# Optimization experiments

Hardware: AMD Instinct MI355X
Metric: run time of the kernel (lower is better)

## Reference

```python
import jax, jax.numpy as jnp
import numpy as np
from jax import lax

R = 4                      # search_range
FILTERS = [128, 128, 96, 64, 32, 2]
B, H, W, C = 8, 128, 128, 128
IN_CH = (2 * R + 1) ** 2 + C + 2   # 81 + 128 + 2 = 211


def mish(x):
    return x * jnp.tanh(jax.nn.softplus(x))


def sepconv(x, dw, pw, b=None, act=True):
    # depthwise 3x3 (SAME) then pointwise 1x1, matching SeparableConv2D
    cin = x.shape[-1]
    y = lax.conv_general_dilated(
        x, dw, window_strides=(1, 1), padding='SAME',
        dimension_numbers=('NHWC', 'HWIO', 'NHWC'),
        feature_group_count=cin)
    y = jnp.einsum('bhwc,co->bhwo', y, pw)
    if b is not None:
        y = y + b
    return mish(y) if act else y


def warp(img, flo):
    # bilinear backward warp; TF casts float->int32 with truncation, jnp matches
    b_, h, w, _ = img.shape
    xs = jnp.arange(w, dtype=jnp.float32)[None, None, :]
    ys = jnp.arange(h, dtype=jnp.float32)[None, :, None]
    x = xs + flo[..., 0]
    y = ys + flo[..., 1]
    x0 = x.astype(jnp.int32)
    y0 = y.astype(jnp.int32)
    x1 = x0 + 1
    y1 = y0 + 1
    x0c = jnp.clip(x0, 0, w - 1)
    x1c = jnp.clip(x1, 0, w - 1)
    y0c = jnp.clip(y0, 0, h - 1)
    y1c = jnp.clip(y1, 0, h - 1)
    bi = jnp.arange(b_)[:, None, None]
    Ia = img[bi, y0c, x0c]
    Ib = img[bi, y1c, x0c]
    Ic = img[bi, y0c, x1c]
    Id = img[bi, y1c, x1c]
    x0f = x0c.astype(jnp.float32); x1f = x1c.astype(jnp.float32)
    y0f = y0c.astype(jnp.float32); y1f = y1c.astype(jnp.float32)
    wa = ((x1f - x) * (y1f - y))[..., None]
    wb = ((x1f - x) * (y - y0f))[..., None]
    wc = ((x - x0f) * (y1f - y))[..., None]
    wd = ((x - x0f) * (y - y0f))[..., None]
    return wa * Ia + wb * Ib + wc * Ic + wd * Id


def cost_volume(prv, nxt):
    _, h, w, _ = prv.shape
    d = 2 * R + 1
    pad = jnp.pad(nxt, ((0, 0), (R, R), (R, R), (0, 0)))
    costs = [jnp.mean(prv * pad[:, i:i + h, j:j + w, :], axis=-1)
             for i in range(d) for j in range(d)]
    return jnp.stack(costs, axis=-1)  # [B,H,W,81]


def setup_inputs() -> dict:
    key = jax.random.key(0)
    ks = iter(jax.random.split(key, 64))
    inp = {
        'prv': jax.random.normal(next(ks), (B, H, W, C), dtype=jnp.float32),
        'nxt': jax.random.normal(next(ks), (B, H, W, C), dtype=jnp.float32),
        'flo': jax.random.normal(next(ks), (B, H, W, 2), dtype=jnp.float32),
    }
    cin = IN_CH
    for i, f in enumerate(FILTERS):
        inp[f'dw{i}'] = 0.05 * jax.random.normal(next(ks), (3, 3, 1, cin), dtype=jnp.float32)
        inp[f'pw{i}'] = 0.05 * jax.random.normal(next(ks), (cin, f), dtype=jnp.float32)
        if i < len(FILTERS) - 1:
            inp[f'b{i}'] = 0.05 * jax.random.normal(next(ks), (f,), dtype=jnp.float32)
        cin = f
    return inp


def reference(prv, nxt, flo,
              dw0, pw0, b0, dw1, pw1, b1, dw2, pw2, b2,
              dw3, pw3, b3, dw4, pw4, b4, dw5, pw5):
    nxt_w = warp(nxt, flo)
    cost = cost_volume(prv, nxt_w)
    x = jnp.concatenate([cost, prv, flo], axis=-1)  # [B,H,W,211]
    x = sepconv(x, dw0, pw0, b0)
    x = sepconv(x, dw1, pw1, b1)
    x = sepconv(x, dw2, pw2, b2)
    x = sepconv(x, dw3, pw3, b3)
    x = sepconv(x, dw4, pw4, b4)
    x = sepconv(x, dw5, pw5, None, act=False)  # final flow, no bias/activation
    return x
```

## Files before the change

kernel.cpp:

```cpp
#include <hip/hip_runtime.h>
#include <hip/hip_bf16.h>

#define B_ 8
#define H_ 128
#define W_ 128
#define C_ 128

using f32x4 = __attribute__((ext_vector_type(4))) float;
using s16x8 = __attribute__((ext_vector_type(8))) short;
using us4   = __attribute__((ext_vector_type(4))) unsigned short;

__device__ __forceinline__ float mish_f(float x) {
    float t = __expf(fminf(x, 20.0f));
    float u = t * (t + 2.0f);
    return x * u / (u + 2.0f);
}

__device__ __forceinline__ int swz_row(int blk) {
    return ((blk & 7) << 7) | (blk >> 3);
}

__device__ __forceinline__ unsigned short f2bf_rne(float x) {
    unsigned u = __builtin_bit_cast(unsigned, x);
    u += 0x7FFFu + ((u >> 16) & 1u);
    return (unsigned short)(u >> 16);
}
__device__ __forceinline__ float bf2f(unsigned short h) {
    unsigned u = ((unsigned)h) << 16;
    return __builtin_bit_cast(float, u);
}
__device__ __forceinline__ unsigned short f2bf_hw(float x) {
    return __bfloat16_as_ushort(__float2bfloat16(x));
}

__device__ __forceinline__ f32x4 load4u(const float* p) {
    f32x4 v;
    __builtin_memcpy(&v, p, 16);
    return v;
}

__global__ __launch_bounds__(256) void warp_kernel(
    const float* __restrict__ nxt, const float* __restrict__ flo,
    float* __restrict__ nxtw)
{
    const int tid = threadIdx.x;
    const int c   = tid & 127;
    const int pix = blockIdx.x * 2 + (tid >> 7);
    const int b   = pix >> 14;
    const int rem = pix & 16383;
    const int y   = rem >> 7;
    const int x   = rem & 127;

    const float fx = flo[(size_t)pix * 2 + 0];
    const float fy = flo[(size_t)pix * 2 + 1];
    const float xf = (float)x + fx;
    const float yf = (float)y + fy;
    const int x0 = (int)xf;
    const int y0 = (int)yf;
    const int x0c = min(max(x0, 0), W_ - 1);
    const int x1c = min(max(x0 + 1, 0), W_ - 1);
    const int y0c = min(max(y0, 0), H_ - 1);
    const int y1c = min(max(y0 + 1, 0), H_ - 1);
    const float x0f = (float)x0c, x1f = (float)x1c;
    const float y0f = (float)y0c, y1f = (float)y1c;
    const float wa = (x1f - xf) * (y1f - yf);
    const float wb = (x1f - xf) * (yf - y0f);
    const float wc = (xf - x0f) * (y1f - yf);
    const float wd = (xf - x0f) * (yf - y0f);

    const float* base = nxt + (size_t)b * H_ * W_ * C_;
    const float Ia = base[((size_t)y0c * W_ + x0c) * C_ + c];
    const float Ib = base[((size_t)y1c * W_ + x0c) * C_ + c];
    const float Ic = base[((size_t)y0c * W_ + x1c) * C_ + c];
    const float Id = base[((size_t)y1c * W_ + x1c) * C_ + c];
    nxtw[(size_t)pix * C_ + c] = wa * Ia + wb * Ib + wc * Ic + wd * Id;
}

__global__ __launch_bounds__(1024, 4) void costvol_mfma_kernel(
    const float* __restrict__ prv, const float* __restrict__ nxtw,
    float* __restrict__ cost)
{
    constexpr int NSTR = 40;
    __shared__ unsigned short Nhi[2][144 * NSTR];
    __shared__ unsigned short Nlo[2][144 * NSTR];
    __shared__ float scr[8][512];

    const int tid  = threadIdx.x;
    const int lane = tid & 63;
    const int wv   = tid >> 6;
    const int w    = wv >> 1;
    const int nt   = wv & 1;
    const int r    = swz_row(blockIdx.x);
    const int y    = r & 127;
    const int b    = r >> 7;
    const int ko   = (lane >> 4) * 8;
    const int m15  = lane & 15;

    auto stageN = [&](int q, int kt, int bb) {
        if (q < 0 || q >= H_) return;
        const float* nb = nxtw + ((size_t)(b * H_ + q) * W_) * C_ + kt * 32;
        #pragma unroll
        for (int p = 0; p < 2; ++p) {
            const int idx = tid + 1024 * p;
            if (p == 0 || tid < 128) {
                const int sm = idx >> 3;
                const int c4 = (idx & 7) * 4;
                const int gx = sm - 8;
                float4 v = make_float4(0.f, 0.f, 0.f, 0.f);
                if (gx >= 0 && gx < W_)
                    v = *(const float4*)&nb[(size_t)gx * C_ + c4];
                us4 hv, lv;
                #pragma unroll
                for (int j = 0; j < 4; ++j) {
                    const float f = ((const float*)&v)[j];
                    const unsigned short hh = f2bf_hw(f);
                    hv[j] = hh;
                    lv[j] = f2bf_hw(f - bf2f(hh));
                }
                *(us4*)&Nhi[bb][sm * NSTR + c4] = hv;
                *(us4*)&Nlo[bb][sm * NSTR + c4] = lv;
            }
        }
    };

    f32x4 acc[9];
    #pragma unroll
    for (int d = 0; d < 9; ++d) acc[d] = (f32x4){0.f, 0.f, 0.f, 0.f};

    const float* pbase = prv + ((size_t)r * W_ + (w * 16 + m15)) * C_;
    float4 pf0 = *(const float4*)&pbase[ko];
    float4 pf1 = *(const float4*)&pbase[ko + 4];

    stageN(y - 4, 0, 0);
    __syncthreads();

    int cur = 0;
    s16x8 ahi, alo;
    for (int kt = 0; kt < 4; ++kt) {
        #pragma unroll
        for (int d = 0; d < 9; ++d) {
            if (d == 0) {
                #pragma unroll
                for (int j = 0; j < 8; ++j) {
                    const float f = (j < 4) ? ((const float*)&pf0)[j]
                                            : ((const float*)&pf1)[j - 4];
                    const unsigned short hh = f2bf_hw(f);
                    ahi[j] = (short)hh;
                    alo[j] = (short)f2bf_hw(f - bf2f(hh));
                }
            }
            if (d == 5 && kt < 3) {
                pf0 = *(const float4*)&pbase[(kt + 1) * 32 + ko];
                pf1 = *(const float4*)&pbase[(kt + 1) * 32 + ko + 4];
            }
            {
                const int nkt = (d == 8) ? kt + 1 : kt;
                const int nd  = (d == 8) ? 0 : d + 1;
                if (nkt < 4) stageN(y + nd - 4, nkt, cur ^ 1);
            }
            const int q = y + d - 4;
            if (q >= 0 && q < H_) {
                const int boff = (w * 16 + nt * 16 + m15) * NSTR + ko;
                const s16x8 bhi = *(const s16x8*)&Nhi[cur][boff];
                const s16x8 blo = *(const s16x8*)&Nlo[cur][boff];
                acc[d] = __builtin_amdgcn_mfma_f32_16x16x32_bf16(alo, bhi, acc[d], 0, 0, 0);
                acc[d] = __builtin_amdgcn_mfma_f32_16x16x32_bf16(ahi, blo, acc[d], 0, 0, 0);
                acc[d] = __builtin_amdgcn_mfma_f32_16x16x32_bf16(ahi, bhi, acc[d], 0, 0, 0);
            }
            __syncthreads();
            cur ^= 1;
        }
    }

    const int quad = lane >> 4;
    #pragma unroll
    for (int d = 0; d < 9; ++d) {
        #pragma unroll
        for (int g = 0; g < 4; ++g)
            scr[w][(quad * 4 + g) * 32 + nt * 16 + m15] = acc[d][g];
        __syncthreads();
        #pragma unroll
        for (int p = 0; p < 2; ++p) {
            const int idx = tid + 1024 * p;
            if (p == 0 || tid < 128) {
                const int x  = idx / 9;
                const int dx = idx - x * 9;
                const int ww = x >> 4, m = x & 15;
                const float v = scr[ww][m * 32 + m + dx + 4] * (1.0f / 128.0f);
                cost[((size_t)r * W_ + x) * 81 + d * 9 + dx] = v;
            }
        }
        __syncthreads();
    }
}

__global__ __launch_bounds__(256) void prep_kernel(
    const float* __restrict__ pw, int CIN, int COUT, int NT,
    unsigned short* __restrict__ hi, unsigned short* __restrict__ lo)
{
    const int kt = blockIdx.x / NT;
    const int nt = blockIdx.x - kt * NT;
    #pragma unroll
    for (int s = 0; s < 2; ++s) {
        const int e = threadIdx.x + 256 * s;
        const int n = e >> 5, k = e & 31;
        const int kg = kt * 32 + k, ng = nt * 16 + n;
        const float v = (kg < CIN && ng < COUT) ? pw[(size_t)kg * COUT + ng] : 0.0f;
        const unsigned short h = f2bf_rne(v);
        const unsigned short l = f2bf_rne(v - bf2f(h));
        const size_t o = ((size_t)blockIdx.x * 16 + n) * 32 + k;
        hi[o] = h; lo[o] = l;
    }
}

template<int CIN, int COUT, bool ACT, bool IS_L0>
__global__ __launch_bounds__(512, 4) void sepconv_kernel(
    const float* __restrict__ in,
    const float* __restrict__ cost, const float* __restrict__ prv,
    const float* __restrict__ flo,
    const float* __restrict__ dw,
    const unsigned short* __restrict__ Bhi, const unsigned short* __restrict__ Blo,
    const float* __restrict__ bias, float* __restrict__ out)
{
    constexpr int KT   = (CIN + 31) / 32;
    constexpr int KPAD = KT * 32;
    constexpr int NT   = (COUT + 15) / 16;
    constexpr int KSTR = 40;
    __shared__ unsigned short Ahi[128 * KSTR];
    __shared__ unsigned short Alo[128 * KSTR];
    __shared__ float dwl[9 * KPAD];

    const int tid  = threadIdx.x;
    const int lane = tid & 63;
    const int w    = tid >> 6;
    const int r    = swz_row(blockIdx.x);
    const int h    = r & 127;
    const int b    = r >> 7;

    const int co = (tid & 7) * 4;
    const int xb = (tid >> 3) * 2;

    bool rowok[3]; int rowpix[3];
    #pragma unroll
    for (int ky = 0; ky < 3; ++ky) {
        const int yy = h + ky - 1;
        rowok[ky]  = (yy >= 0) && (yy < H_);
        rowpix[ky] = (b * H_ + (rowok[ky] ? yy : h)) * W_;
    }

    for (int i = tid; i < 9 * KPAD; i += 512) {
        const int t = i / KPAD, c = i - t * KPAD;
        dwl[i] = (c < CIN) ? dw[t * CIN + c] : 0.0f;
    }

    f32x4 acc[NT];
    #pragma unroll
    for (int n = 0; n < NT; ++n)
        acc[n] = (f32x4){0.0f, 0.0f, 0.0f, 0.0f};

    __syncthreads();

    for (int kt = 0; kt < KT; ++kt) {
        const int cg = kt * 32 + co;
        f32x4 V[3][4];
        #pragma unroll
        for (int ky = 0; ky < 3; ++ky) {
            #pragma unroll
            for (int xm = 0; xm < 4; ++xm) {
                const int xx = xb - 1 + xm;
                f32x4 v = (f32x4){0.f, 0.f, 0.f, 0.f};
                if (rowok[ky] && xx >= 0 && xx < W_) {
                    const int px = rowpix[ky] + xx;
                    if constexpr (IS_L0) {
                        if (cg <= 76) {
                            v = load4u(cost + (size_t)px * 81 + cg);
                        } else if (cg == 80) {
                            const float* cp = cost + (size_t)px * 81;
                            const float* pp = prv + (size_t)px * 128;
                            v = (f32x4){cp[80], pp[0], pp[1], pp[2]};
                        } else if (cg <= 204) {
                            v = load4u(prv + (size_t)px * 128 + (cg - 81));
                        } else if (cg == 208) {
                            const float* pp = prv + (size_t)px * 128;
                            const float* fp = flo + (size_t)px * 2;
                            v = (f32x4){pp[127], fp[0], fp[1], 0.f};
                        }
                    } else {
                        v = *(const f32x4*)(in + (size_t)px * CIN + cg);
                    }
                }
                V[ky][xm] = v;
            }
        }

        f32x4 a0 = (f32x4){0.f, 0.f, 0.f, 0.f};
        f32x4 a1 = (f32x4){0.f, 0.f, 0.f, 0.f};
        #pragma unroll
        for (int ky = 0; ky < 3; ++ky) {
            #pragma unroll
            for (int kx = 0; kx < 3; ++kx) {
                const f32x4 wv = *(const f32x4*)&dwl[(ky * 3 + kx) * KPAD + cg - kt * 32 + kt * 32];
                a0 += wv * V[ky][kx];
                a1 += wv * V[ky][kx + 1];
            }
        }

        us4 h0, l0, h1, l1;
        #pragma unroll
        for (int j = 0; j < 4; ++j) {
            const unsigned short hh0 = f2bf_hw(a0[j]);
            h0[j] = hh0; l0[j] = f2bf_hw(a0[j] - bf2f(hh0));
            const unsigned short hh1 = f2bf_hw(a1[j]);
            h1[j] = hh1; l1[j] = f2bf_hw(a1[j] - bf2f(hh1));
        }

        __syncthreads();
        *(us4*)&Ahi[(xb + 0) * KSTR + co] = h0;
        *(us4*)&Ahi[(xb + 1) * KSTR + co] = h1;
        *(us4*)&Alo[(xb + 0) * KSTR + co] = l0;
        *(us4*)&Alo[(xb + 1) * KSTR + co] = l1;
        __syncthreads();

        const int mrow = w * 16 + (lane & 15);
        const int ko   = (lane >> 4) * 8;
        const s16x8 ahi = *(const s16x8*)&Ahi[mrow * KSTR + ko];
        const s16x8 alo = *(const s16x8*)&Alo[mrow * KSTR + ko];
        #pragma unroll
        for (int nt = 0; nt < NT; ++nt) {
            const size_t boff = (((size_t)(kt * NT + nt)) * 16 + (lane & 15)) * 32
                              + (size_t)ko;
            const s16x8 bhi = *(const s16x8*)&Bhi[boff];
            const s16x8 blo = *(const s16x8*)&Blo[boff];
            acc[nt] = __builtin_amdgcn_mfma_f32_16x16x32_bf16(alo, bhi, acc[nt], 0, 0, 0);
            acc[nt] = __builtin_amdgcn_mfma_f32_16x16x32_bf16(ahi, blo, acc[nt], 0, 0, 0);
            acc[nt] = __builtin_amdgcn_mfma_f32_16x16x32_bf16(ahi, bhi, acc[nt], 0, 0, 0);
        }
    }

    const int n    = lane & 15;
    const int quad = lane >> 4;
    #pragma unroll
    for (int nt = 0; nt < NT; ++nt) {
        const int o = nt * 16 + n;
        if ((COUT % 16 == 0) || (o < COUT)) {
            const float bv = ACT ? bias[o] : 0.0f;
            #pragma unroll
            for (int reg = 0; reg < 4; ++reg) {
                const int px = w * 16 + quad * 4 + reg;
                const float v = acc[nt][reg] + bv;
                out[((size_t)r * W_ + px) * COUT + o] = ACT ? mish_f(v) : v;
            }
        }
    }
}

extern "C" void kernel_launch(void* const* d_in, const int* in_sizes, int n_in,
                              void* d_out, int out_size, void* d_ws, size_t ws_size,
                              hipStream_t stream)
{
    (void)in_sizes; (void)n_in; (void)out_size; (void)ws_size;
    const float* prv = (const float*)d_in[0];
    const float* nxt = (const float*)d_in[1];
    const float* flo = (const float*)d_in[2];
    const float* dw0 = (const float*)d_in[3];
    const float* pw0 = (const float*)d_in[4];
    const float* b0  = (const float*)d_in[5];
    const float* dw1 = (const float*)d_in[6];
    const float* pw1 = (const float*)d_in[7];
    const float* b1  = (const float*)d_in[8];
    const float* dw2 = (const float*)d_in[9];
    const float* pw2 = (const float*)d_in[10];
    const float* b2  = (const float*)d_in[11];
    const float* dw3 = (const float*)d_in[12];
    const float* pw3 = (const float*)d_in[13];
    const float* b3  = (const float*)d_in[14];
    const float* dw4 = (const float*)d_in[15];
    const float* pw4 = (const float*)d_in[16];
    const float* b4  = (const float*)d_in[17];
    const float* dw5 = (const float*)d_in[18];
    const float* pw5 = (const float*)d_in[19];

    char* ws = (char*)d_ws;
    float* bufA = (float*)ws;
    float* bufC = (float*)(ws + 67108864);
    float* costb = bufC;
    float* l4out = (float*)(ws + 67108864 + 33554432);
    float* outp  = (float*)d_out;

    unsigned short* W0h = (unsigned short*)(ws + 112000000);
    unsigned short* W0l = (unsigned short*)(ws + 112000000 + 57344);
    unsigned short* W1h = (unsigned short*)d_out;
    unsigned short* W1l = (unsigned short*)d_out + 16384;
    unsigned short* W2h = (unsigned short*)(ws + 50331648);
    unsigned short* W2l = (unsigned short*)(ws + 50356224);
    unsigned short* W3h = (unsigned short*)(ws + 50380800);
    unsigned short* W3l = (unsigned short*)(ws + 50393088);
    unsigned short* W4h = (unsigned short*)(ws + 50405376);
    unsigned short* W4l = (unsigned short*)(ws + 50409472);
    unsigned short* W5h = (unsigned short*)(ws + 50413568);
    unsigned short* W5l = (unsigned short*)(ws + 50414592);

    const float* nullf = nullptr;

    warp_kernel<<<65536, 256, 0, stream>>>(nxt, flo, bufA);
    costvol_mfma_kernel<<<1024, 1024, 0, stream>>>(prv, bufA, costb);

    prep_kernel<<<7 * 8, 256, 0, stream>>>(pw0, 211, 128, 8, W0h, W0l);
    prep_kernel<<<4 * 8, 256, 0, stream>>>(pw1, 128, 128, 8, W1h, W1l);

    sepconv_kernel<211, 128, true,  true ><<<1024, 512, 0, stream>>>(
        nullf, costb, prv, flo, dw0, W0h, W0l, b0, bufA);
    sepconv_kernel<128, 128, true,  false><<<1024, 512, 0, stream>>>(
        bufA, nullf, nullf, nullf, dw1, W1h, W1l, b1, bufC);

    prep_kernel<<<4 * 6, 256, 0, stream>>>(pw2, 128,  96, 6, W2h, W2l);
    prep_kernel<<<3 * 4, 256, 0, stream>>>(pw3,  96,  64, 4, W3h, W3l);
    prep_kernel<<<2 * 2, 256, 0, stream>>>(pw4,  64,  32, 2, W4h, W4l);
    prep_kernel<<<1 * 1, 256, 0, stream>>>(pw5,  32,   2, 1, W5h, W5l);

    sepconv_kernel<128,  96, true,  false><<<1024, 512, 0, stream>>>(
        bufC, nullf, nullf, nullf, dw2, W2h, W2l, b2, bufA);
    sepconv_kernel< 96,  64, true,  false><<<1024, 512, 0, stream>>>(
        bufA, nullf, nullf, nullf, dw3, W3h, W3l, b3, bufC);
    sepconv_kernel< 64,  32, true,  false><<<1024, 512, 0, stream>>>(
        bufC, nullf, nullf, nullf, dw4, W4h, W4l, b4, l4out);
    sepconv_kernel< 32,   2, false, false><<<1024, 512, 0, stream>>>(
        l4out, nullf, nullf, nullf, dw5, W5h, W5l, nullf, outp);
}
```

Baseline: 590.1 us.

## Emit split-bf16 warped image and read cost-volume operands directly from global

The warp kernel now writes the warped image as hi/lo bf16 halves instead of fp32, so the split is computed once rather than redone in every cost-volume block. The cost-volume kernel drops its double-buffered LDS staging and per-step barriers and loads MFMA B operands straight from global memory (L2/L1 cached). The epilogue uses a padded scratch layout with per-wave stores to cut bank conflicts and barriers. The risk is more global/L2 traffic per MFMA and exposed load latency without LDS reuse across the 9 row offsets.

```diff
diff --git a/kernel.cpp b/kernel.cpp
--- a/kernel.cpp
+++ b/kernel.cpp
@@ -41,7 +41,7 @@
 
 __global__ __launch_bounds__(256) void warp_kernel(
     const float* __restrict__ nxt, const float* __restrict__ flo,
-    float* __restrict__ nxtw)
+    unsigned short* __restrict__ nwh, unsigned short* __restrict__ nwl)
 {
     const int tid = threadIdx.x;
     const int c   = tid & 127;
@@ -73,17 +73,21 @@
     const float Ib = base[((size_t)y1c * W_ + x0c) * C_ + c];
     const float Ic = base[((size_t)y0c * W_ + x1c) * C_ + c];
     const float Id = base[((size_t)y1c * W_ + x1c) * C_ + c];
-    nxtw[(size_t)pix * C_ + c] = wa * Ia + wb * Ib + wc * Ic + wd * Id;
+    const float v  = wa * Ia + wb * Ib + wc * Ic + wd * Id;
+
+    const unsigned short h = f2bf_hw(v);
+    const unsigned short l = f2bf_hw(v - bf2f(h));
+    nwh[(size_t)pix * C_ + c] = h;
+    nwl[(size_t)pix * C_ + c] = l;
 }
 
 __global__ __launch_bounds__(1024, 4) void costvol_mfma_kernel(
-    const float* __restrict__ prv, const float* __restrict__ nxtw,
+    const float* __restrict__ prv,
+    const unsigned short* __restrict__ nwh,
+    const unsigned short* __restrict__ nwl,
     float* __restrict__ cost)
 {
-    constexpr int NSTR = 40;
-    __shared__ unsigned short Nhi[2][144 * NSTR];
-    __shared__ unsigned short Nlo[2][144 * NSTR];
-    __shared__ float scr[8][512];
+    __shared__ float scr[8][576];
 
     const int tid  = threadIdx.x;
     const int lane = tid & 63;
@@ -93,104 +97,69 @@
     const int r    = swz_row(blockIdx.x);
     const int y    = r & 127;
     const int b    = r >> 7;
+    const int m15  = lane & 15;
     const int ko   = (lane >> 4) * 8;
-    const int m15  = lane & 15;
-
-    auto stageN = [&](int q, int kt, int bb) {
-        if (q < 0 || q >= H_) return;
-        const float* nb = nxtw + ((size_t)(b * H_ + q) * W_) * C_ + kt * 32;
-        #pragma unroll
-        for (int p = 0; p < 2; ++p) {
-            const int idx = tid + 1024 * p;
-            if (p == 0 || tid < 128) {
-                const int sm = idx >> 3;
-                const int c4 = (idx & 7) * 4;
-                const int gx = sm - 8;
-                float4 v = make_float4(0.f, 0.f, 0.f, 0.f);
-                if (gx >= 0 && gx < W_)
-                    v = *(const float4*)&nb[(size_t)gx * C_ + c4];
-                us4 hv, lv;
-                #pragma unroll
-                for (int j = 0; j < 4; ++j) {
-                    const float f = ((const float*)&v)[j];
-                    const unsigned short hh = f2bf_hw(f);
-                    hv[j] = hh;
-                    lv[j] = f2bf_hw(f - bf2f(hh));
-                }
-                *(us4*)&Nhi[bb][sm * NSTR + c4] = hv;
-                *(us4*)&Nlo[bb][sm * NSTR + c4] = lv;
-            }
-        }
-    };
+
+    const int  xs   = (w + nt) * 16 + m15 - 8;
+    const bool xok  = (xs >= 0) && (xs < W_);
+    const int  xoff = (xok ? xs : 0) * C_ + ko;
 
     f32x4 acc[9];
     #pragma unroll
     for (int d = 0; d < 9; ++d) acc[d] = (f32x4){0.f, 0.f, 0.f, 0.f};
 
-    const float* pbase = prv + ((size_t)r * W_ + (w * 16 + m15)) * C_;
-    float4 pf0 = *(const float4*)&pbase[ko];
-    float4 pf1 = *(const float4*)&pbase[ko + 4];
-
-    stageN(y - 4, 0, 0);
-    __syncthreads();
-
-    int cur = 0;
-    s16x8 ahi, alo;
+    const float* pbase = prv + ((size_t)r * W_ + (w * 16 + m15)) * C_ + ko;
+
     for (int kt = 0; kt < 4; ++kt) {
+        const f32x4 p0 = *(const f32x4*)(pbase + kt * 32);
+        const f32x4 p1 = *(const f32x4*)(pbase + kt * 32 + 4);
+        s16x8 ahi, alo;
+        #pragma unroll
+        for (int j = 0; j < 8; ++j) {
+            const float f = (j < 4) ? p0[j] : p1[j - 4];
+            const unsigned short hh = f2bf_hw(f);
+            ahi[j] = (short)hh;
+            alo[j] = (short)f2bf_hw(f - bf2f(hh));
+        }
+
+        const size_t kb = (size_t)kt * 32 + xoff;
         #pragma unroll
         for (int d = 0; d < 9; ++d) {
-            if (d == 0) {
-                #pragma unroll
-                for (int j = 0; j < 8; ++j) {
-                    const float f = (j < 4) ? ((const float*)&pf0)[j]
-                                            : ((const float*)&pf1)[j - 4];
-                    const unsigned short hh = f2bf_hw(f);
-                    ahi[j] = (short)hh;
-                    alo[j] = (short)f2bf_hw(f - bf2f(hh));
-                }
-            }
-            if (d == 5 && kt < 3) {
-                pf0 = *(const float4*)&pbase[(kt + 1) * 32 + ko];
-                pf1 = *(const float4*)&pbase[(kt + 1) * 32 + ko + 4];
-            }
-            {
-                const int nkt = (d == 8) ? kt + 1 : kt;
-                const int nd  = (d == 8) ? 0 : d + 1;
-                if (nkt < 4) stageN(y + nd - 4, nkt, cur ^ 1);
-            }
             const int q = y + d - 4;
             if (q >= 0 && q < H_) {
-                const int boff = (w * 16 + nt * 16 + m15) * NSTR + ko;
-                const s16x8 bhi = *(const s16x8*)&Nhi[cur][boff];
-                const s16x8 blo = *(const s16x8*)&Nlo[cur][boff];
+                const size_t off = ((size_t)(b * H_ + q) * W_) * C_ + kb;
+                s16x8 bhi = (s16x8){0,0,0,0,0,0,0,0};
+                s16x8 blo = (s16x8){0,0,0,0,0,0,0,0};
+                if (xok) {
+                    bhi = *(const s16x8*)(nwh + off);
+                    blo = *(const s16x8*)(nwl + off);
+                }
                 acc[d] = __builtin_amdgcn_mfma_f32_16x16x32_bf16(alo, bhi, acc[d], 0, 0, 0);
                 acc[d] = __builtin_amdgcn_mfma_f32_16x16x32_bf16(ahi, blo, acc[d], 0, 0, 0);
                 acc[d] = __builtin_amdgcn_mfma_f32_16x16x32_bf16(ahi, bhi, acc[d], 0, 0, 0);
             }
-            __syncthreads();
-            cur ^= 1;
         }
     }
 
     const int quad = lane >> 4;
     #pragma unroll
     for (int d = 0; d < 9; ++d) {
+        __syncthreads();
         #pragma unroll
         for (int g = 0; g < 4; ++g)
-            scr[w][(quad * 4 + g) * 32 + nt * 16 + m15] = acc[d][g];
+            scr[w][(quad * 4 + g) * 36 + nt * 16 + m15] = acc[d][g];
         __syncthreads();
         #pragma unroll
         for (int p = 0; p < 2; ++p) {
-            const int idx = tid + 1024 * p;
-            if (p == 0 || tid < 128) {
-                const int x  = idx / 9;
-                const int dx = idx - x * 9;
-                const int ww = x >> 4, m = x & 15;
-                const float v = scr[ww][m * 32 + m + dx + 4] * (1.0f / 128.0f);
-                cost[((size_t)r * W_ + x) * 81 + d * 9 + dx] = v;
+            const int local = lane + 64 * p;
+            if (local < 72) {
+                const int idx = nt * 72 + local;
+                const int xl  = idx / 9;
+                const int dx  = idx - xl * 9;
+                const float v = scr[w][xl * 37 + dx + 4] * (1.0f / 128.0f);
+                cost[((size_t)r * W_ + (w * 16 + xl)) * 81 + d * 9 + dx] = v;
             }
         }
-        __syncthreads();
     }
 }
 
@@ -299,7 +268,7 @@
         for (int ky = 0; ky < 3; ++ky) {
             #pragma unroll
             for (int kx = 0; kx < 3; ++kx) {
-                const f32x4 wv = *(const f32x4*)&dwl[(ky * 3 + kx) * KPAD + cg - kt * 32 + kt * 32];
+                const f32x4 wv = *(const f32x4*)&dwl[(ky * 3 + kx) * KPAD + cg];
                 a0 += wv * V[ky][kx];
                 a1 += wv * V[ky][kx + 1];
             }
@@ -387,6 +356,9 @@
     float* l4out = (float*)(ws + 67108864 + 33554432);
     float* outp  = (float*)d_out;
 
+    unsigned short* nwh = (unsigned short*)ws;
+    unsigned short* nwl = (unsigned short*)(ws + 33554432);
+
     unsigned short* W0h = (unsigned short*)(ws + 112000000);
     unsigned short* W0l = (unsigned short*)(ws + 112000000 + 57344);
     unsigned short* W1h = (unsigned short*)d_out;
@@ -402,8 +374,8 @@
 
     const float* nullf = nullptr;
 
-    warp_kernel<<<65536, 256, 0, stream>>>(nxt, flo, bufA);
-    costvol_mfma_kernel<<<1024, 1024, 0, stream>>>(prv, bufA, costb);
+    warp_kernel<<<65536, 256, 0, stream>>>(nxt, flo, nwh, nwl);
+    costvol_mfma_kernel<<<1024, 1024, 0, stream>>>(prv, nwh, nwl, costb);
 
     prep_kernel<<<7 * 8, 256, 0, stream>>>(pw0, 211, 128, 8, W0h, W0l);
     prep_kernel<<<4 * 8, 256, 0, stream>>>(pw1, 128, 128, 8, W1h, W1l);
```

After: 633.5 us. 1.07x slower.
